# Kernel optimization log

Hardware: AMD Instinct MI355X
Metric: run time of the kernel (lower is better)

The kernel has to match this reference:

```python
import jax, jax.numpy as jnp
import numpy as np

N, E, B = 50000, 100000, 512   # nodes, edges, graphs
H, F_NODE, F_EDGE, T_OUT = 64, 16, 8, 1
T = 3                           # message-passing steps


def setup_inputs() -> dict:
    key = jax.random.key(0)
    ks = jax.random.split(key, 18)

    def w(k, shape, fan_in):
        return jax.random.normal(k, shape, dtype=jnp.float32) / np.sqrt(fan_in)

    return {
        "node_features": jax.random.normal(ks[0], (N, F_NODE), dtype=jnp.float32),
        "edge_features": jax.random.normal(ks[1], (E, F_EDGE), dtype=jnp.float32),
        "Esrc": jax.random.randint(ks[2], (E,), 0, N, dtype=jnp.int32),
        "Etgt": jax.random.randint(ks[3], (E,), 0, N, dtype=jnp.int32),
        "batch": jnp.sort(jax.random.randint(ks[4], (N,), 0, B, dtype=jnp.int32)),
        # input linear: node_features -> hidden
        "Win": w(ks[5], (H, F_NODE), F_NODE),
        "bin_": jnp.zeros((H,), jnp.float32),
        # edge encoder MLP: edge_features -> hidden -> hidden*hidden
        "We1": w(ks[6], (H, F_EDGE), F_EDGE),
        "be1": jnp.zeros((H,), jnp.float32),
        "We2": w(ks[7], (H * H, H), H),
        "be2": jnp.zeros((H * H,), jnp.float32),
        # GRU cell (shared across T steps)
        "Wih": w(ks[8], (3 * H, H), H),
        "bih": jnp.zeros((3 * H,), jnp.float32),
        "Whh": w(ks[9], (3 * H, H), H),
        "bhh": jnp.zeros((3 * H,), jnp.float32),
        # output linear: hidden -> target_features
        "Wout": w(ks[10], (T_OUT, H), H),
        "bout": jnp.zeros((T_OUT,), jnp.float32),
    }


def _gru(x, h, Wih, bih, Whh, bhh):
    gi = x @ Wih.T + bih            # [N, 3H]
    gh = h @ Whh.T + bhh
    i_r, i_z, i_n = jnp.split(gi, 3, axis=-1)
    h_r, h_z, h_n = jnp.split(gh, 3, axis=-1)
    r = jax.nn.sigmoid(i_r + h_r)
    z = jax.nn.sigmoid(i_z + h_z)
    n = jnp.tanh(i_n + r * h_n)
    return (1.0 - z) * n + z * h


def reference(node_features, edge_features, Esrc, Etgt, batch,
              Win, bin_, We1, be1, We2, be2,
              Wih, bih, Whh, bhh, Wout, bout):
    # Edge encoder MLP -> per-edge [H, H] message matrix (ENN style)
    eh = jax.nn.relu(edge_features @ We1.T + be1)          # [E, H]
    edge_data = (eh @ We2.T + be2).reshape(E, H, H)        # [E, H, H]

    x = node_features @ Win.T + bin_                       # [N, H]

    for _ in range(T):  # small fixed layer count
        msg = jnp.einsum('eij,ej->ei', edge_data, x[Esrc])  # per-edge matvec
        agg = jax.ops.segment_sum(msg, Etgt, num_segments=N)
        x = _gru(agg, x, Wih, bih, Whh, bhh)

    out = x @ Wout.T + bout                                # [N, 1]
    pooled = jax.ops.segment_sum(out, batch, num_segments=B)  # [B, 1]
    return pooled
```

## Files before the change

### kernel.cpp

```cpp
#include <hip/hip_runtime.h>
#include <hip/hip_fp16.h>

#define NN 50000
#define NE 100000
#define NB 512

typedef _Float16 f16x8 __attribute__((ext_vector_type(8)));
typedef float f32x4  __attribute__((ext_vector_type(4)));

__device__ __forceinline__ float sigm(float v) { return 1.0f / (1.0f + __expf(-v)); }
__device__ __forceinline__ float tanh_fast(float v) {
    float e = __expf(-2.0f * fabsf(v));
    float t = (1.0f - e) / (1.0f + e);
    return v < 0.f ? -t : t;
}

__global__ __launch_bounds__(256) void node_in_kernel(
    const float* __restrict__ nf, const float* __restrict__ Win,
    const float* __restrict__ bin_, float* __restrict__ x, __half* __restrict__ xh)
{
    int idx = blockIdx.x * 256 + threadIdx.x;
    if (idx >= NN * 64) return;
    int n = idx >> 6, h = idx & 63;
    float acc = bin_[h];
    #pragma unroll
    for (int f = 0; f < 16; f++) acc += nf[n * 16 + f] * Win[h * 16 + f];
    x[idx] = acc;
    xh[idx] = __float2half(acc);
}

__global__ __launch_bounds__(256) void edge_l1_kernel(
    const float* __restrict__ ef, const float* __restrict__ We1,
    const float* __restrict__ be1, __half* __restrict__ ehh)
{
    int idx = blockIdx.x * 256 + threadIdx.x;
    if (idx >= NE * 64) return;
    int e = idx >> 6, k = idx & 63;
    float acc = be1[k];
    #pragma unroll
    for (int f = 0; f < 8; f++) acc += ef[e * 8 + f] * We1[k * 8 + f];
    ehh[idx] = __float2half(fmaxf(acc, 0.0f));
}

__global__ __launch_bounds__(256) void pack_b_kernel(
    const float* __restrict__ We2, const float* __restrict__ be2,
    __half* __restrict__ Bp)
{
    int idx = blockIdx.x * 256 + threadIdx.x;
    if (idx >= 130 * 2048) return;
    int i  = idx & 7;
    int l  = (idx >> 3) & 63;
    int nt = (idx >> 9) & 3;
    int kt = idx >> 11;
    int n  = nt * 16 + (l & 15);
    int kk = (l >> 4) * 8 + i;
    int p  = kt * 32 + kk;
    float v;
    if (p < 4096) {
        int j = p >> 6, k = p & 63;
        v = We2[((size_t)(n * 64 + j)) * 64 + k];
    } else {
        v = be2[n * 64 + (p - 4096)];
    }
    Bp[idx] = __float2half(v);
}

__global__ __launch_bounds__(256) void pack_gru_kernel(
    const float* __restrict__ Wih, const float* __restrict__ Whh,
    __half* __restrict__ WG)
{
    int idx = blockIdx.x * 256 + threadIdx.x;
    if (idx >= 24576) return;
    int kk = idx & 31;
    int n  = (idx >> 5) & 15;
    int nt = (idx >> 9) % 24;
    int kt = (idx >> 9) / 24;
    int k = kt * 32 + kk;
    int col192 = (nt % 12) * 16 + n;
    int gate = col192 >> 6, h = col192 & 63;
    const float* src = (nt < 12) ? Wih : Whh;
    WG[idx] = __float2half(src[((size_t)(gate * 64 + h)) * 64 + k]);
}

__global__ __launch_bounds__(256, 3) void msg_kernel(
    const __half* __restrict__ xh, const __half* __restrict__ ehh,
    const __half* __restrict__ Bp,
    const int* __restrict__ Esrc, const int* __restrict__ Etgt,
    float* __restrict__ agg)
{
    __shared__ __half xs[4][32][72];
    __shared__ __half bbuf[2][4096];
    __shared__ int tgt_s[128];
    const int tid = threadIdx.x;
    const int e0 = blockIdx.x * 128;
    const int w = tid >> 6, lane = tid & 63;
    const int m = lane & 15, quad = lane >> 4;

    {
        const int r = tid >> 1, part = tid & 1;
        const int e = e0 + r;
        const bool ok = (e < NE);
        const int src = ok ? Esrc[e] : 0;
        if (part == 0) tgt_s[r] = ok ? Etgt[e] : -1;
        const uint4* xsrc = (const uint4*)(xh + (size_t)src * 64 + part * 32);
        __half* dst = &xs[r >> 5][r & 31][part * 32];
        #pragma unroll
        for (int i = 0; i < 4; i++) {
            uint4 v = ok ? xsrc[i] : make_uint4(0, 0, 0, 0);
            *(uint4*)(dst + i * 8) = v;
        }
    }

    {
        const uint4* s = (const uint4*)Bp;
        uint4 v0 = s[tid], v1 = s[256 + tid];
        ((uint4*)bbuf[0])[tid] = v0;
        ((uint4*)bbuf[0])[256 + tid] = v1;
    }

    __half2 ehc2[2][2][4];
    #pragma unroll
    for (int mt = 0; mt < 2; mt++) {
        const int e = e0 + w * 32 + mt * 16 + m;
        if (e < NE) {
            union { uint4 u; __half2 h[4]; } u0, u1;
            u0.u = *(const uint4*)(ehh + (size_t)e * 64 + quad * 8);
            u1.u = *(const uint4*)(ehh + (size_t)e * 64 + 32 + quad * 8);
            #pragma unroll
            for (int q = 0; q < 4; q++) { ehc2[mt][0][q] = u0.h[q]; ehc2[mt][1][q] = u1.h[q]; }
        } else {
            __half2 z = __halves2half2(__float2half(0.f), __float2half(0.f));
            #pragma unroll
            for (int q = 0; q < 4; q++) { ehc2[mt][0][q] = z; ehc2[mt][1][q] = z; }
        }
    }

    f32x4 acc[2][4];
    #pragma unroll
    for (int a = 0; a < 2; a++)
        #pragma unroll
        for (int b = 0; b < 4; b++)
            #pragma unroll
            for (int q = 0; q < 4; q++) acc[a][b][q] = 0.f;

    __syncthreads();

    int cur = 0;
    #pragma unroll 1
    for (int j = 0; j < 64; j++) {
        const uint4* s = (const uint4*)(Bp + (size_t)(j + 1) * 4096);
        uint4 p0 = s[tid];
        uint4 p1 = s[256 + tid];

        __half2 xsj2[2];
        #pragma unroll
        for (int mt = 0; mt < 2; mt++) {
            __half v = xs[w][mt * 16 + m][j];
            xsj2[mt] = __halves2half2(v, v);
        }
        #pragma unroll
        for (int half = 0; half < 2; half++) {
            f16x8 bf[4];
            #pragma unroll
            for (int nt = 0; nt < 4; nt++)
                bf[nt] = *(const f16x8*)(&bbuf[cur][half * 2048 + nt * 512 + lane * 8]);
            #pragma unroll
            for (int mt = 0; mt < 2; mt++) {
                union { __half2 h[4]; f16x8 v; } u;
                #pragma unroll
                for (int q = 0; q < 4; q++)
                    u.h[q] = __hmul2(xsj2[mt], ehc2[mt][half][q]);
                #pragma unroll
                for (int nt = 0; nt < 4; nt++)
                    acc[mt][nt] = __builtin_amdgcn_mfma_f32_16x16x32_f16(
                        u.v, bf[nt], acc[mt][nt], 0, 0, 0);
            }
        }

        uint4* d = (uint4*)bbuf[cur ^ 1];
        d[tid] = p0;
        d[256 + tid] = p1;
        __syncthreads();
        cur ^= 1;
    }

    #pragma unroll
    for (int half = 0; half < 2; half++) {
        f16x8 bf[4];
        #pragma unroll
        for (int nt = 0; nt < 4; nt++)
            bf[nt] = *(const f16x8*)(&bbuf[cur][half * 2048 + nt * 512 + lane * 8]);
        #pragma unroll
        for (int mt = 0; mt < 2; mt++) {
            f16x8 af = *(const f16x8*)(&xs[w][mt * 16 + m][half * 32 + quad * 8]);
            #pragma unroll
            for (int nt = 0; nt < 4; nt++)
                acc[mt][nt] = __builtin_amdgcn_mfma_f32_16x16x32_f16(
                    af, bf[nt], acc[mt][nt], 0, 0, 0);
        }
    }

    #pragma unroll
    for (int mt = 0; mt < 2; mt++) {
        #pragma unroll
        for (int r = 0; r < 4; r++) {
            const int row = w * 32 + mt * 16 + quad * 4 + r;
            const int t = tgt_s[row];
            if (t >= 0) {
                #pragma unroll
                for (int nt = 0; nt < 4; nt++)
                    atomicAdd(agg + (size_t)t * 64 + nt * 16 + m, acc[mt][nt][r]);
            }
        }
    }
}

__global__ __launch_bounds__(256, 3) void gru_kernel(
    const float* __restrict__ agg, float* __restrict__ x, __half* __restrict__ xh,
    const __half* __restrict__ WG,
    const float* __restrict__ bih, const float* __restrict__ bhh)
{
    __shared__ __half wlds[24576];
    const int tid = threadIdx.x;
    {
        const uint4* src = (const uint4*)WG;
        uint4* dst = (uint4*)wlds;
        #pragma unroll
        for (int i = 0; i < 12; i++) dst[i * 256 + tid] = src[i * 256 + tid];
    }
    __syncthreads();

    const int w = tid >> 6, lane = tid & 63, m = lane & 15, quad = lane >> 4;
    const int nbase = blockIdx.x * 64 + w * 16;
    const int anode = nbase + m;
    const bool aok = (anode < NN);

    f16x8 a_agg[2], a_x[2];
    #pragma unroll
    for (int kt = 0; kt < 2; kt++) {
        const int koff = kt * 32 + quad * 8;
        if (aok) {
            const float* ap = agg + (size_t)anode * 64 + koff;
            float4 f0 = *(const float4*)ap;
            float4 f1 = *(const float4*)(ap + 4);
            union { __half2 h[4]; f16x8 v; } u;
            u.h[0] = __floats2half2_rn(f0.x, f0.y);
            u.h[1] = __floats2half2_rn(f0.z, f0.w);
            u.h[2] = __floats2half2_rn(f1.x, f1.y);
            u.h[3] = __floats2half2_rn(f1.z, f1.w);
            a_agg[kt] = u.v;
            a_x[kt] = *(const f16x8*)(xh + (size_t)anode * 64 + koff);
        } else {
            f16x8 z;
            #pragma unroll
            for (int i = 0; i < 8; i++) z[i] = (_Float16)0;
            a_agg[kt] = z; a_x[kt] = z;
        }
    }

    f32x4 acc[24];
    #pragma unroll
    for (int nt = 0; nt < 24; nt++)
        #pragma unroll
        for (int q = 0; q < 4; q++) acc[nt][q] = 0.f;

    #pragma unroll
    for (int kt = 0; kt < 2; kt++) {
        #pragma unroll
        for (int nt = 0; nt < 24; nt++) {
            f16x8 b = *(const f16x8*)(wlds + (kt * 24 + nt) * 512 + m * 32 + quad * 8);
            acc[nt] = __builtin_amdgcn_mfma_f32_16x16x32_f16(
                (nt < 12) ? a_agg[kt] : a_x[kt], b, acc[nt], 0, 0, 0);
        }
    }

    #pragma unroll
    for (int t = 0; t < 4; t++) {
        const int h = t * 16 + m;
        const float bir = bih[h], biz = bih[64 + h], bin = bih[128 + h];
        const float bhr = bhh[h], bhz = bhh[64 + h], bhn = bhh[128 + h];
        #pragma unroll
        for (int r = 0; r < 4; r++) {
            const int nd = nbase + quad * 4 + r;
            if (nd >= NN) continue;
            float ir  = acc[t][r]      + bir;
            float iz  = acc[4 + t][r]  + biz;
            float in_ = acc[8 + t][r]  + bin;
            float hr  = acc[12 + t][r] + bhr;
            float hz  = acc[16 + t][r] + bhz;
            float hn  = acc[20 + t][r] + bhn;
            float rg = sigm(ir + hr);
            float z  = sigm(iz + hz);
            float n  = tanh_fast(in_ + rg * hn);
            float xold = x[(size_t)nd * 64 + h];
            float xn = (1.0f - z) * n + z * xold;
            x[(size_t)nd * 64 + h] = xn;
            xh[(size_t)nd * 64 + h] = __float2half(xn);
        }
    }
}

__global__ __launch_bounds__(256) void pool_kernel(
    const float* __restrict__ x, const float* __restrict__ Wout,
    const float* __restrict__ bout, const int* __restrict__ batch,
    float* __restrict__ out)
{
    const int node = blockIdx.x * 256 + threadIdx.x;
    if (node >= NN) return;
    float acc = bout[0];
    const float4* xp = (const float4*)(x + (size_t)node * 64);
    #pragma unroll
    for (int i = 0; i < 16; i++) {
        float4 v = xp[i];
        acc += v.x * Wout[4*i] + v.y * Wout[4*i+1] + v.z * Wout[4*i+2] + v.w * Wout[4*i+3];
    }
    atomicAdd(out + batch[node], acc);
}

extern "C" void kernel_launch(void* const* d_in, const int* in_sizes, int n_in,
                              void* d_out, int out_size, void* d_ws, size_t ws_size,
                              hipStream_t stream)
{
    const float* nf   = (const float*)d_in[0];
    const float* ef   = (const float*)d_in[1];
    const int*   Esrc = (const int*)  d_in[2];
    const int*   Etgt = (const int*)  d_in[3];
    const int*   bat  = (const int*)  d_in[4];
    const float* Win  = (const float*)d_in[5];
    const float* bin_ = (const float*)d_in[6];
    const float* We1  = (const float*)d_in[7];
    const float* be1  = (const float*)d_in[8];
    const float* We2  = (const float*)d_in[9];
    const float* be2  = (const float*)d_in[10];
    const float* Wih  = (const float*)d_in[11];
    const float* bih  = (const float*)d_in[12];
    const float* Whh  = (const float*)d_in[13];
    const float* bhh  = (const float*)d_in[14];
    const float* Wout = (const float*)d_in[15];
    const float* bout = (const float*)d_in[16];

    char* ws = (char*)d_ws;
    float*  x   = (float*)(ws);
    float*  agg = (float*)(ws + 12800000);
    __half* xh  = (__half*)(ws + 25600000);
    __half* ehh = (__half*)(ws + 32000000);
    __half* Bp  = (__half*)(ws + 44800000);
    __half* WG  = (__half*)(ws + 45400064);

    hipMemsetAsync(d_out, 0, NB * sizeof(float), stream);

    node_in_kernel<<<(NN * 64 + 255) / 256, 256, 0, stream>>>(nf, Win, bin_, x, xh);
    edge_l1_kernel<<<(NE * 64 + 255) / 256, 256, 0, stream>>>(ef, We1, be1, ehh);
    pack_b_kernel<<<(130 * 2048 + 255) / 256, 256, 0, stream>>>(We2, be2, Bp);
    pack_gru_kernel<<<(24576 + 255) / 256, 256, 0, stream>>>(Wih, Whh, WG);

    for (int t = 0; t < 3; t++) {
        hipMemsetAsync(agg, 0, (size_t)NN * 64 * sizeof(float), stream);
        msg_kernel<<<(NE + 127) / 128, 256, 0, stream>>>(xh, ehh, Bp, Esrc, Etgt, agg);
        gru_kernel<<<(NN + 63) / 64, 256, 0, stream>>>(agg, x, xh, WG, bih, bhh);
    }

    pool_kernel<<<(NN + 255) / 256, 256, 0, stream>>>(x, Wout, bout, bat, (float*)d_out);
}
```

Before: 472.5 us.

## Replace atomic scatter-add with CSR-ordered message buffer and segmented reduce in GRU

Builds a CSR ordering of edges by target node (histogram, single-block scan, scatter of per-edge slot indices). The message kernel now writes each edge's message to its sorted slot instead of doing float atomicAdds, and the GRU kernel sums each node's contiguous message range into shared memory before the gate matmuls. This removes the per-step agg memset and atomic contention. In exchange it adds a 25.6MB message buffer, three preprocessing kernels (one of them a single-block scan), and a serial per-node gather loop that lowers the GRU kernel's occupancy hint.

```diff
diff --git a/kernel.cpp b/kernel.cpp
--- a/kernel.cpp
+++ b/kernel.cpp
@@ -82,15 +82,66 @@
     WG[idx] = __float2half(src[((size_t)(gate * 64 + h)) * 64 + k]);
 }
 
+
+__global__ __launch_bounds__(256) void hist_kernel(
+    const int* __restrict__ Etgt, int* __restrict__ cnt)
+{
+    int e = blockIdx.x * 256 + threadIdx.x;
+    if (e < NE) atomicAdd(&cnt[Etgt[e]], 1);
+}
+
+__global__ __launch_bounds__(1024) void scan_kernel(
+    const int* __restrict__ cnt, int* __restrict__ off, int* __restrict__ wpos)
+{
+    __shared__ int part[1024];
+    const int tid = threadIdx.x;
+    const int CH = (NN + 1023) / 1024;
+    const int base = tid * CH;
+    int s = 0;
+    for (int i = 0; i < CH; i++) {
+        int idx = base + i;
+        if (idx < NN) s += cnt[idx];
+    }
+    part[tid] = s;
+    __syncthreads();
+    for (int d = 1; d < 1024; d <<= 1) {
+        int u = (tid >= d) ? part[tid - d] : 0;
+        int v = part[tid];
+        __syncthreads();
+        part[tid] = v + u;
+        __syncthreads();
+    }
+    int run = (tid > 0) ? part[tid - 1] : 0;
+    for (int i = 0; i < CH; i++) {
+        int idx = base + i;
+        if (idx < NN) {
+            off[idx] = run;
+            wpos[idx] = run;
+            run += cnt[idx];
+        }
+    }
+    if (tid == 0) off[NN] = part[1023];
+}
+
+__global__ __launch_bounds__(256) void scatter_kernel(
+    const int* __restrict__ Etgt, int* __restrict__ wpos, int* __restrict__ inv)
+{
+    int e = blockIdx.x * 256 + threadIdx.x;
+    if (e < NE) {
+        int p = atomicAdd(&wpos[Etgt[e]], 1);
+        inv[e] = p;
+    }
+}
+
 __global__ __launch_bounds__(256, 3) void msg_kernel(
     const __half* __restrict__ xh, const __half* __restrict__ ehh,
     const __half* __restrict__ Bp,
-    const int* __restrict__ Esrc, const int* __restrict__ Etgt,
-    float* __restrict__ agg)
+    const int* __restrict__ Esrc, const int* __restrict__ inv,
+    float* __restrict__ msgf)
 {
     __shared__ __half xs[4][32][72];
     __shared__ __half bbuf[2][4096];
-    __shared__ int tgt_s[128];
+    __shared__ int inv_s[128];
     const int tid = threadIdx.x;
     const int e0 = blockIdx.x * 128;
     const int w = tid >> 6, lane = tid & 63;
@@ -101,7 +152,7 @@
         const int e = e0 + r;
         const bool ok = (e < NE);
         const int src = ok ? Esrc[e] : 0;
-        if (part == 0) tgt_s[r] = ok ? Etgt[e] : -1;
+        if (part == 0) inv_s[r] = ok ? inv[e] : 0;
         const uint4* xsrc = (const uint4*)(xh + (size_t)src * 64 + part * 32);
         __half* dst = &xs[r >> 5][r & 31][part * 32];
         #pragma unroll
@@ -205,22 +256,25 @@
         #pragma unroll
         for (int r = 0; r < 4; r++) {
             const int row = w * 32 + mt * 16 + quad * 4 + r;
-            const int t = tgt_s[row];
-            if (t >= 0) {
+            const int e = e0 + row;
+            if (e < NE) {
+                const size_t base = (size_t)inv_s[row] * 64 + m;
                 #pragma unroll
                 for (int nt = 0; nt < 4; nt++)
-                    atomicAdd(agg + (size_t)t * 64 + nt * 16 + m, acc[mt][nt][r]);
+                    msgf[base + nt * 16] = acc[mt][nt][r];
             }
         }
     }
 }
 
-__global__ __launch_bounds__(256, 3) void gru_kernel(
-    const float* __restrict__ agg, float* __restrict__ x, __half* __restrict__ xh,
+__global__ __launch_bounds__(256, 2) void gru_kernel(
+    const float* __restrict__ msgf, const int* __restrict__ off,
+    float* __restrict__ x, __half* __restrict__ xh,
     const __half* __restrict__ WG,
     const float* __restrict__ bih, const float* __restrict__ bhh)
 {
     __shared__ __half wlds[24576];
+    __shared__ float aggs[64][68];
     const int tid = threadIdx.x;
     {
         const uint4* src = (const uint4*)WG;
@@ -228,10 +282,23 @@
         #pragma unroll
         for (int i = 0; i < 12; i++) dst[i * 256 + tid] = src[i * 256 + tid];
     }
+
+    const int w = tid >> 6, lane = tid & 63, m = lane & 15, quad = lane >> 4;
+    const int nb0 = blockIdx.x * 64;
+
+    for (int i = 0; i < 16; i++) {
+        const int node = nb0 + w * 16 + i;
+        float s = 0.f;
+        if (node < NN) {
+            const int b = off[node], eN = off[node + 1];
+            for (int p = b; p < eN; p++)
+                s += msgf[(size_t)p * 64 + lane];
+        }
+        aggs[w * 16 + i][lane] = s;
+    }
     __syncthreads();
 
-    const int w = tid >> 6, lane = tid & 63, m = lane & 15, quad = lane >> 4;
-    const int nbase = blockIdx.x * 64 + w * 16;
+    const int nbase = nb0 + w * 16;
     const int anode = nbase + m;
     const bool aok = (anode < NN);
 
@@ -239,8 +306,8 @@
     #pragma unroll
     for (int kt = 0; kt < 2; kt++) {
         const int koff = kt * 32 + quad * 8;
-        if (aok) {
-            const float* ap = agg + (size_t)anode * 64 + koff;
+        {
+            const float* ap = &aggs[w * 16 + m][koff];
             float4 f0 = *(const float4*)ap;
             float4 f1 = *(const float4*)(ap + 4);
             union { __half2 h[4]; f16x8 v; } u;
@@ -249,12 +316,14 @@
             u.h[2] = __floats2half2_rn(f1.x, f1.y);
             u.h[3] = __floats2half2_rn(f1.z, f1.w);
             a_agg[kt] = u.v;
+        }
+        if (aok) {
             a_x[kt] = *(const f16x8*)(xh + (size_t)anode * 64 + koff);
         } else {
             f16x8 z;
             #pragma unroll
             for (int i = 0; i < 8; i++) z[i] = (_Float16)0;
-            a_agg[kt] = z; a_x[kt] = z;
+            a_x[kt] = z;
         }
     }
 
@@ -340,24 +409,32 @@
     const float* bout = (const float*)d_in[16];
 
     char* ws = (char*)d_ws;
-    float*  x   = (float*)(ws);
-    float*  agg = (float*)(ws + 12800000);
-    __half* xh  = (__half*)(ws + 25600000);
-    __half* ehh = (__half*)(ws + 32000000);
-    __half* Bp  = (__half*)(ws + 44800000);
-    __half* WG  = (__half*)(ws + 45400064);
+    float*  x    = (float*)(ws);
+    float*  msgf = (float*)(ws + 12800000);
+    __half* xh   = (__half*)(ws + 38400000);
+    __half* ehh  = (__half*)(ws + 44800000);
+    __half* Bp   = (__half*)(ws + 57600000);
+    __half* WG   = (__half*)(ws + 58132480);
+    int*    cnt  = (int*)   (ws + 58181632);
+    int*    off  = (int*)   (ws + 58381648);
+    int*    wpos = (int*)   (ws + 58581664);
+    int*    inv  = (int*)   (ws + 58781680);
 
     hipMemsetAsync(d_out, 0, NB * sizeof(float), stream);
+    hipMemsetAsync(cnt, 0, (NN + 1) * sizeof(int), stream);
 
     node_in_kernel<<<(NN * 64 + 255) / 256, 256, 0, stream>>>(nf, Win, bin_, x, xh);
     edge_l1_kernel<<<(NE * 64 + 255) / 256, 256, 0, stream>>>(ef, We1, be1, ehh);
     pack_b_kernel<<<(130 * 2048 + 255) / 256, 256, 0, stream>>>(We2, be2, Bp);
     pack_gru_kernel<<<(24576 + 255) / 256, 256, 0, stream>>>(Wih, Whh, WG);
 
+    hist_kernel<<<(NE + 255) / 256, 256, 0, stream>>>(Etgt, cnt);
+    scan_kernel<<<1, 1024, 0, stream>>>(cnt, off, wpos);
+    scatter_kernel<<<(NE + 255) / 256, 256, 0, stream>>>(Etgt, wpos, inv);
+
     for (int t = 0; t < 3; t++) {
-        hipMemsetAsync(agg, 0, (size_t)NN * 64 * sizeof(float), stream);
-        msg_kernel<<<(NE + 127) / 128, 256, 0, stream>>>(xh, ehh, Bp, Esrc, Etgt, agg);
-        gru_kernel<<<(NN + 63) / 64, 256, 0, stream>>>(agg, x, xh, WG, bih, bhh);
+        msg_kernel<<<(NE + 127) / 128, 256, 0, stream>>>(xh, ehh, Bp, Esrc, inv, msgf);
+        gru_kernel<<<(NN + 63) / 64, 256, 0, stream>>>(msgf, off, x, xh, WG, bih, bhh);
     }
 
     pool_kernel<<<(NN + 255) / 256, 256, 0, stream>>>(x, Wout, bout, bat, (float*)d_out);
```

New measurement: 646.8 us. 36.9% more time.
